# Kernel tuning notes

Hardware: AMD Instinct MI355X
Metric: run time of the kernel (lower is better)

The kernel has to match this reference:

```python
import jax, jax.numpy as jnp
import numpy as np

A, B, S, AD, H, NH = 8, 32768, 128, 16, 64, 4
D = H // NH  # attend_dim = 16
MAX_ACTION = 1.0


def setup_inputs() -> dict:
    key = jax.random.key(0)
    ks = jax.random.split(key, 16)
    sc = 0.05
    return {
        'states': jax.random.normal(ks[0], (A, B, S), jnp.float32),
        'actions': jax.random.normal(ks[1], (A, B, AD), jnp.float32),
        'Ws': jax.random.normal(ks[2], (S, H), jnp.float32) * sc,
        'bs': jnp.zeros((H,), jnp.float32),
        'We': jax.random.normal(ks[3], (S + AD, H), jnp.float32) * sc,
        'be': jnp.zeros((H,), jnp.float32),
        'Wk': jax.random.normal(ks[4], (NH, H, D), jnp.float32) * sc,
        'Wsel': jax.random.normal(ks[5], (NH, H, D), jnp.float32) * sc,
        'Wv': jax.random.normal(ks[6], (NH, H, D), jnp.float32) * sc,
        'bv': jnp.zeros((NH, D), jnp.float32),
        'W1': jax.random.normal(ks[7], (2 * H, H), jnp.float32) * sc,
        'b1': jnp.zeros((H,), jnp.float32),
        'W2': jax.random.normal(ks[8], (H, 1), jnp.float32) * sc,
        'b2': jnp.zeros((1,), jnp.float32),
    }


def reference(states, actions, Ws, bs, We, be, Wk, Wsel, Wv, bv, W1, b1, W2, b2):
    # per-agent encoders (shared params, as in the torch module)
    s_enc = jax.nn.relu(jnp.einsum('abs,sh->abh', states, Ws) + bs)          # [A,B,H]
    sa = jnp.concatenate([states, actions / MAX_ACTION], axis=-1)            # [A,B,S+AD]
    sa_enc = jax.nn.relu(jnp.einsum('abi,ih->abh', sa, We) + be)             # [A,B,H]

    # per-head keys / values / selectors (n = head axis)
    keys = jnp.einsum('abh,nhd->nabd', sa_enc, Wk)                           # [NH,A,B,D]
    vals = jax.nn.relu(jnp.einsum('abh,nhd->nabd', sa_enc, Wv) + bv[:, None, None, :])
    sel = jnp.einsum('abh,nhd->nabd', s_enc, Wsel)                           # [NH,A,B,D]

    # exclude-self attention over agents == masked softmax over agent axis j
    logits = jnp.einsum('nibd,njbd->nibj', sel, keys) / jnp.sqrt(jnp.float32(D))
    self_mask = jnp.eye(A, dtype=bool)                                       # [A(i),A(j)]
    logits = jnp.where(self_mask[None, :, None, :], -1e9, logits)
    w = jax.nn.softmax(logits, axis=-1)                                      # [NH,A,B,A]
    other = jnp.einsum('nibj,njbd->nibd', w, vals)                           # [NH,A,B,D]
    other_cat = jnp.transpose(other, (1, 2, 0, 3)).reshape(A, B, NH * D)     # [A,B,H]

    critic_in = jnp.concatenate([sa_enc, other_cat], axis=-1)                # [A,B,2H]
    h = jax.nn.relu(jnp.einsum('abi,ih->abh', critic_in, W1) + b1)
    q = jnp.einsum('abh,ho->abo', h, W2) + b2                                # [A,B,1]
    return q
```

## Files before the change

### kernel.cpp

```cpp
#include <hip/hip_runtime.h>
#include <hip/hip_bf16.h>

#define A_N 8
#define B_N 32768
#define S_N 128
#define AD_N 16

typedef __attribute__((ext_vector_type(8))) short short8;
typedef __attribute__((ext_vector_type(4))) float floatx4;

#define MFMA16(a, b, c) __builtin_amdgcn_mfma_f32_16x16x32_bf16(a, b, c, 0, 0, 0)

__device__ __forceinline__ short f2bf(float f) {
    __hip_bfloat16 h = __float2bfloat16(f);
    return *reinterpret_cast<short*>(&h);
}
__device__ __forceinline__ float bf2f(short s) {
    return __uint_as_float(((unsigned)(unsigned short)s) << 16);
}
__device__ __forceinline__ void pk2(short8& r, int i, float a, float b) {
    __hip_bfloat162 p = __float22bfloat162_rn(make_float2(a, b));
    short2 s = *reinterpret_cast<short2*>(&p);
    r[i] = s.x; r[i + 1] = s.y;
}
__device__ __forceinline__ short8 cvt8(float4 x0, float4 x1) {
    short8 r;
    pk2(r, 0, x0.x, x0.y); pk2(r, 2, x0.z, x0.w);
    pk2(r, 4, x1.x, x1.y); pk2(r, 6, x1.z, x1.w);
    return r;
}
__device__ __forceinline__ void wait_lgkm() {
    asm volatile("s_waitcnt lgkmcnt(0)" ::: "memory");
}
__device__ __forceinline__ void lds_barrier() {
    asm volatile("s_waitcnt lgkmcnt(0)\ns_barrier" ::: "memory");
}

#define W_TOTAL 41472
#define OFF_Ws 10240
#define OFF_Wk 18944
#define OFF_Wsel 23552
#define OFF_Wv 28160
#define OFF_W1 32768

__global__ void prep_weights(const float* __restrict__ Ws, const float* __restrict__ We,
                             const float* __restrict__ Wk, const float* __restrict__ Wsel,
                             const float* __restrict__ Wv, const float* __restrict__ W1,
                             short* __restrict__ w) {
    int idx = blockIdx.x * 256 + threadIdx.x;
    if (idx >= W_TOTAL) return;
    float v;
    if (idx < OFF_Ws)        { int n = idx / 160, k = idx % 160; v = (k < 144) ? We[k * 64 + n] : 0.f; }
    else if (idx < OFF_Wk)   { int i = idx - OFF_Ws;  int n = i / 136, k = i % 136; v = (k < 128) ? Ws[k * 64 + n] : 0.f; }
    else if (idx < OFF_Wsel) { int i = idx - OFF_Wk;  int n = i / 72,  k = i % 72;  v = (k < 64) ? Wk[(n >> 4) * 1024 + k * 16 + (n & 15)] : 0.f; }
    else if (idx < OFF_Wv)   { int i = idx - OFF_Wsel;int n = i / 72,  k = i % 72;  v = (k < 64) ? Wsel[(n >> 4) * 1024 + k * 16 + (n & 15)] : 0.f; }
    else if (idx < OFF_W1)   { int i = idx - OFF_Wv;  int n = i / 72,  k = i % 72;  v = (k < 64) ? Wv[(n >> 4) * 1024 + k * 16 + (n & 15)] : 0.f; }
    else                     { int i = idx - OFF_W1;  int n = i / 136, k = i % 136; v = (k < 128) ? W1[k * 64 + n] : 0.f; }
    w[idx] = f2bf(v);
}

#define ST 72
#define OFF_Eb 41472
#define OFF_Tb 50688
#define OFF_Kb 59904
#define OFF_Vb 69120
#define SMEM_TOT 78336

#define TILES 4

__global__ __launch_bounds__(512, 2)
void attention_critic_mfma(
    const float* __restrict__ states, const float* __restrict__ actions,
    const float* __restrict__ bs, const float* __restrict__ be,
    const float* __restrict__ bv, const float* __restrict__ b1,
    const float* __restrict__ W2, const float* __restrict__ b2,
    const short* __restrict__ wts, float* __restrict__ out)
{
    __shared__ __align__(16) short smem[SMEM_TOT];
    short* lWe   = smem;
    short* lWs   = smem + OFF_Ws;
    short* lWk   = smem + OFF_Wk;
    short* lWsel = smem + OFF_Wsel;
    short* lWv   = smem + OFF_Wv;
    short* lW1   = smem + OFF_W1;
    short* Eb    = smem + OFF_Eb;
    short* Tb    = smem + OFF_Tb;
    short* Kb    = smem + OFF_Kb;
    short* Vb    = smem + OFF_Vb;

    const int tid  = threadIdx.x;
    const int wv   = tid >> 6;
    const int lane = tid & 63;
    const int lq   = lane >> 4;
    const int ln   = lane & 15;
    const int rA   = wv * 16 + ln;
    const int bbase = blockIdx.x * (TILES * 16);

    for (int c = wv; c < 81; c += 8) {
        const unsigned int* g = reinterpret_cast<const unsigned int*>(wts + c * 512) + lane * 4;
        __builtin_amdgcn_global_load_lds(g, reinterpret_cast<unsigned int*>(smem + c * 512), 16, 0, 0);
    }

    const float* srow = states  + ((long)wv * B_N + bbase + ln) * S_N;
    const float* arow = actions + ((long)wv * B_N + bbase + ln) * AD_N;

    float4 ps[8]; float4 pa[2];
    #pragma unroll
    for (int s = 0; s < 4; ++s) {
        ps[2 * s]     = *reinterpret_cast<const float4*>(srow + s * 32 + lq * 8);
        ps[2 * s + 1] = *reinterpret_cast<const float4*>(srow + s * 32 + lq * 8 + 4);
    }
    if (lq < 2) {
        pa[0] = *reinterpret_cast<const float4*>(arow + lq * 8);
        pa[1] = *reinterpret_cast<const float4*>(arow + lq * 8 + 4);
    }
    __syncthreads();

    const floatx4 z = {0.f, 0.f, 0.f, 0.f};

    #pragma unroll 1
    for (int t = 0; t < TILES; ++t) {
        const int b0 = bbase + t * 16;

        floatx4 accE[4] = {z, z, z, z};
        floatx4 accS[4] = {z, z, z, z};
        #pragma unroll
        for (int s = 0; s < 4; ++s) {
            const int kk = s * 32 + lq * 8;
            short8 af = cvt8(ps[2 * s], ps[2 * s + 1]);
            #pragma unroll
            for (int nt = 0; nt < 4; ++nt) {
                short8 bE = *reinterpret_cast<const short8*>(lWe + (nt * 16 + ln) * 160 + kk);
                short8 bS = *reinterpret_cast<const short8*>(lWs + (nt * 16 + ln) * 136 + kk);
                accE[nt] = MFMA16(af, bE, accE[nt]);
                accS[nt] = MFMA16(af, bS, accS[nt]);
            }
        }
        {
            const int kk = 128 + lq * 8;
            short8 af = {0, 0, 0, 0, 0, 0, 0, 0};
            if (lq < 2) af = cvt8(pa[0], pa[1]);
            #pragma unroll
            for (int nt = 0; nt < 4; ++nt) {
                short8 bE = *reinterpret_cast<const short8*>(lWe + (nt * 16 + ln) * 160 + kk);
                accE[nt] = MFMA16(af, bE, accE[nt]);
            }
        }

        if (t + 1 < TILES) {
            srow += 16 * S_N; arow += 16 * AD_N;
            #pragma unroll
            for (int s = 0; s < 4; ++s) {
                ps[2 * s]     = *reinterpret_cast<const float4*>(srow + s * 32 + lq * 8);
                ps[2 * s + 1] = *reinterpret_cast<const float4*>(srow + s * 32 + lq * 8 + 4);
            }
            if (lq < 2) {
                pa[0] = *reinterpret_cast<const float4*>(arow + lq * 8);
                pa[1] = *reinterpret_cast<const float4*>(arow + lq * 8 + 4);
            }
        }

        #pragma unroll
        for (int nt = 0; nt < 4; ++nt) {
            const int col = nt * 16 + ln;
            const float bE = be[col], bS = bs[col];
            #pragma unroll
            for (int i = 0; i < 4; ++i) {
                const int row = wv * 16 + lq * 4 + i;
                Eb[row * ST + col] = f2bf(fmaxf(accE[nt][i] + bE, 0.f));
                Tb[row * ST + col] = f2bf(fmaxf(accS[nt][i] + bS, 0.f));
            }
        }
        wait_lgkm();

        floatx4 accSel[4] = {z, z, z, z};
        #pragma unroll
        for (int s = 0; s < 2; ++s) {
            short8 af = *reinterpret_cast<const short8*>(Tb + rA * ST + s * 32 + lq * 8);
            #pragma unroll
            for (int nt = 0; nt < 4; ++nt)
                accSel[nt] = MFMA16(af, *reinterpret_cast<const short8*>(lWsel + (nt * 16 + ln) * 72 + s * 32 + lq * 8), accSel[nt]);
        }
        #pragma unroll
        for (int nt = 0; nt < 4; ++nt)
            #pragma unroll
            for (int i = 0; i < 4; ++i)
                Tb[(wv * 16 + lq * 4 + i) * ST + nt * 16 + ln] = f2bf(accSel[nt][i]);

        floatx4 accK[4] = {z, z, z, z}, accV[4] = {z, z, z, z};
        #pragma unroll
        for (int s = 0; s < 2; ++s) {
            short8 af = *reinterpret_cast<const short8*>(Eb + rA * ST + s * 32 + lq * 8);
            #pragma unroll
            for (int nt = 0; nt < 4; ++nt) {
                accK[nt] = MFMA16(af, *reinterpret_cast<const short8*>(lWk + (nt * 16 + ln) * 72 + s * 32 + lq * 8), accK[nt]);
                accV[nt] = MFMA16(af, *reinterpret_cast<const short8*>(lWv + (nt * 16 + ln) * 72 + s * 32 + lq * 8), accV[nt]);
            }
        }
        #pragma unroll
        for (int nt = 0; nt < 4; ++nt) {
            const int col = nt * 16 + ln;
            const float bV = bv[col];
            #pragma unroll
            for (int i = 0; i < 4; ++i) {
                const int row = wv * 16 + lq * 4 + i;
                Kb[row * ST + col] = f2bf(accK[nt][i]);
                Vb[row * ST + col] = f2bf(fmaxf(accV[nt][i] + bV, 0.f));
            }
        }
        lds_barrier();

        {
            const int r3 = tid >> 2, hn = tid & 3;
            const int a3 = r3 >> 4, bl3 = r3 & 15;
            const int co = hn * 16;
            float selv[16];
            short8 s0 = *reinterpret_cast<const short8*>(Tb + r3 * ST + co);
            short8 s1 = *reinterpret_cast<const short8*>(Tb + r3 * ST + co + 8);
            #pragma unroll
            for (int d = 0; d < 8; ++d) { selv[d] = bf2f(s0[d]); selv[d + 8] = bf2f(s1[d]); }
            float lg[8];
            #pragma unroll
            for (int j = 0; j < 8; ++j) {
                const int rj = j * 16 + bl3;
                short8 k0 = *reinterpret_cast<const short8*>(Kb + rj * ST + co);
                short8 k1 = *reinterpret_cast<const short8*>(Kb + rj * ST + co + 8);
                float acc = 0.f;
                #pragma unroll
                for (int d = 0; d < 8; ++d) acc += selv[d] * bf2f(k0[d]) + selv[d + 8] * bf2f(k1[d]);
                lg[j] = (j == a3) ? -1e9f : acc * 0.25f;
            }
            float m = lg[0];
            #pragma unroll
            for (int j = 1; j < 8; ++j) m = fmaxf(m, lg[j]);
            float e[8], ssum = 0.f;
            #pragma unroll
            for (int j = 0; j < 8; ++j) { e[j] = __expf(lg[j] - m); ssum += e[j]; }
            const float inv = 1.f / ssum;
            float oth[16];
            #pragma unroll
            for (int d = 0; d < 16; ++d) oth[d] = 0.f;
            #pragma unroll
            for (int j = 0; j < 8; ++j) {
                const float wj = e[j] * inv;
                const int rj = j * 16 + bl3;
                short8 v0 = *reinterpret_cast<const short8*>(Vb + rj * ST + co);
                short8 v1 = *reinterpret_cast<const short8*>(Vb + rj * ST + co + 8);
                #pragma unroll
                for (int d = 0; d < 8; ++d) { oth[d] += wj * bf2f(v0[d]); oth[d + 8] += wj * bf2f(v1[d]); }
            }
            short8 o0, o1;
            #pragma unroll
            for (int d = 0; d < 8; ++d) { o0[d] = f2bf(oth[d]); o1[d] = f2bf(oth[d + 8]); }
            *reinterpret_cast<short8*>(Tb + r3 * ST + co)     = o0;
            *reinterpret_cast<short8*>(Tb + r3 * ST + co + 8) = o1;
        }
        wait_lgkm();

        floatx4 accH[4] = {z, z, z, z};
        #pragma unroll
        for (int s = 0; s < 4; ++s) {
            short8 af = (s < 2)
                ? *reinterpret_cast<const short8*>(Eb + rA * ST + s * 32 + lq * 8)
                : *reinterpret_cast<const short8*>(Tb + rA * ST + (s - 2) * 32 + lq * 8);
            #pragma unroll
            for (int nt = 0; nt < 4; ++nt)
                accH[nt] = MFMA16(af, *reinterpret_cast<const short8*>(lW1 + (nt * 16 + ln) * 136 + s * 32 + lq * 8), accH[nt]);
        }
        float p0 = 0.f, p1 = 0.f, p2 = 0.f, p3 = 0.f;
        #pragma unroll
        for (int nt = 0; nt < 4; ++nt) {
            const int col = nt * 16 + ln;
            const float w2v = W2[col], bb = b1[col];
            p0 += fmaxf(accH[nt][0] + bb, 0.f) * w2v;
            p1 += fmaxf(accH[nt][1] + bb, 0.f) * w2v;
            p2 += fmaxf(accH[nt][2] + bb, 0.f) * w2v;
            p3 += fmaxf(accH[nt][3] + bb, 0.f) * w2v;
        }
        #pragma unroll
        for (int mk = 1; mk < 16; mk <<= 1) {
            p0 += __shfl_xor(p0, mk, 64);
            p1 += __shfl_xor(p1, mk, 64);
            p2 += __shfl_xor(p2, mk, 64);
            p3 += __shfl_xor(p3, mk, 64);
        }
        if (ln == 0) {
            const float b2v = b2[0];
            float pr[4] = {p0, p1, p2, p3};
            #pragma unroll
            for (int i = 0; i < 4; ++i)
                out[(long)wv * B_N + b0 + lq * 4 + i] = pr[i] + b2v;
        }
        lds_barrier();
    }
}

extern "C" void kernel_launch(void* const* d_in, const int* in_sizes, int n_in,
                              void* d_out, int out_size, void* d_ws, size_t ws_size,
                              hipStream_t stream) {
    const float* states  = (const float*)d_in[0];
    const float* actions = (const float*)d_in[1];
    const float* Ws      = (const float*)d_in[2];
    const float* bs      = (const float*)d_in[3];
    const float* We      = (const float*)d_in[4];
    const float* be      = (const float*)d_in[5];
    const float* Wk      = (const float*)d_in[6];
    const float* Wsel    = (const float*)d_in[7];
    const float* Wv      = (const float*)d_in[8];
    const float* bv      = (const float*)d_in[9];
    const float* W1      = (const float*)d_in[10];
    const float* b1      = (const float*)d_in[11];
    const float* W2      = (const float*)d_in[12];
    const float* b2      = (const float*)d_in[13];
    short* wts = (short*)d_ws;
    float* out = (float*)d_out;

    prep_weights<<<(W_TOTAL + 255) / 256, 256, 0, stream>>>(Ws, We, Wk, Wsel, Wv, W1, wts);
    attention_critic_mfma<<<B_N / (TILES * 16), 512, 0, stream>>>(
        states, actions, bs, be, bv, b1, W2, b2, wts, out);
}
```

Before: 260.5 us.

## Remap rows so each wave holds all agents, removing block-wide barriers

Each wave's 16 rows now cover all 8 agents for 2 batch items, instead of 16 batch items of one agent. The attention step then reads only that wave's own K/V/sel rows, so the two s_barrier calls per tile become per-wave lgkm waits. The We row stride in LDS is also padded from 160 to 168, likely to reduce LDS bank conflicts. The cost is scattered global loads and stores, since each row now touches a different agent's memory region, giving less contiguous access per wave.

```diff
diff --git a/kernel.cpp b/kernel.cpp
--- a/kernel.cpp
+++ b/kernel.cpp
@@ -32,16 +32,13 @@
 __device__ __forceinline__ void wait_lgkm() {
     asm volatile("s_waitcnt lgkmcnt(0)" ::: "memory");
 }
-__device__ __forceinline__ void lds_barrier() {
-    asm volatile("s_waitcnt lgkmcnt(0)\ns_barrier" ::: "memory");
-}
-
-#define W_TOTAL 41472
-#define OFF_Ws 10240
-#define OFF_Wk 18944
-#define OFF_Wsel 23552
-#define OFF_Wv 28160
-#define OFF_W1 32768
+
+#define OFF_Ws 10752
+#define OFF_Wk 19456
+#define OFF_Wsel 24064
+#define OFF_Wv 28672
+#define OFF_W1 33280
+#define W_TOTAL 41984
 
 __global__ void prep_weights(const float* __restrict__ Ws, const float* __restrict__ We,
                              const float* __restrict__ Wk, const float* __restrict__ Wsel,
@@ -50,7 +47,7 @@
     int idx = blockIdx.x * 256 + threadIdx.x;
     if (idx >= W_TOTAL) return;
     float v;
-    if (idx < OFF_Ws)        { int n = idx / 160, k = idx % 160; v = (k < 144) ? We[k * 64 + n] : 0.f; }
+    if (idx < OFF_Ws)        { int n = idx / 168, k = idx % 168; v = (k < 144) ? We[k * 64 + n] : 0.f; }
     else if (idx < OFF_Wk)   { int i = idx - OFF_Ws;  int n = i / 136, k = i % 136; v = (k < 128) ? Ws[k * 64 + n] : 0.f; }
     else if (idx < OFF_Wsel) { int i = idx - OFF_Wk;  int n = i / 72,  k = i % 72;  v = (k < 64) ? Wk[(n >> 4) * 1024 + k * 16 + (n & 15)] : 0.f; }
     else if (idx < OFF_Wv)   { int i = idx - OFF_Wsel;int n = i / 72,  k = i % 72;  v = (k < 64) ? Wsel[(n >> 4) * 1024 + k * 16 + (n & 15)] : 0.f; }
@@ -60,11 +57,11 @@
 }
 
 #define ST 72
-#define OFF_Eb 41472
-#define OFF_Tb 50688
-#define OFF_Kb 59904
-#define OFF_Vb 69120
-#define SMEM_TOT 78336
+#define OFF_Eb 41984
+#define OFF_Tb 51200
+#define OFF_Kb 60416
+#define OFF_Vb 69632
+#define SMEM_TOT 78848
 
 #define TILES 4
 
@@ -96,13 +93,15 @@
     const int rA   = wv * 16 + ln;
     const int bbase = blockIdx.x * (TILES * 16);
 
-    for (int c = wv; c < 81; c += 8) {
+    for (int c = wv; c < 82; c += 8) {
         const unsigned int* g = reinterpret_cast<const unsigned int*>(wts + c * 512) + lane * 4;
         __builtin_amdgcn_global_load_lds(g, reinterpret_cast<unsigned int*>(smem + c * 512), 16, 0, 0);
     }
 
-    const float* srow = states  + ((long)wv * B_N + bbase + ln) * S_N;
-    const float* arow = actions + ((long)wv * B_N + bbase + ln) * AD_N;
+    const int aA  = ln & 7;
+    const int blA = ln >> 3;
+    const float* srow = states  + ((long)aA * B_N + bbase + wv * 2 + blA) * S_N;
+    const float* arow = actions + ((long)aA * B_N + bbase + wv * 2 + blA) * AD_N;
 
     float4 ps[8]; float4 pa[2];
     #pragma unroll
@@ -130,7 +129,7 @@
             short8 af = cvt8(ps[2 * s], ps[2 * s + 1]);
             #pragma unroll
             for (int nt = 0; nt < 4; ++nt) {
-                short8 bE = *reinterpret_cast<const short8*>(lWe + (nt * 16 + ln) * 160 + kk);
+                short8 bE = *reinterpret_cast<const short8*>(lWe + (nt * 16 + ln) * 168 + kk);
                 short8 bS = *reinterpret_cast<const short8*>(lWs + (nt * 16 + ln) * 136 + kk);
                 accE[nt] = MFMA16(af, bE, accE[nt]);
                 accS[nt] = MFMA16(af, bS, accS[nt]);
@@ -142,7 +141,7 @@
             if (lq < 2) af = cvt8(pa[0], pa[1]);
             #pragma unroll
             for (int nt = 0; nt < 4; ++nt) {
-                short8 bE = *reinterpret_cast<const short8*>(lWe + (nt * 16 + ln) * 160 + kk);
+                short8 bE = *reinterpret_cast<const short8*>(lWe + (nt * 16 + ln) * 168 + kk);
                 accE[nt] = MFMA16(af, bE, accE[nt]);
             }
         }
@@ -208,21 +207,23 @@
                 Vb[row * ST + col] = f2bf(fmaxf(accV[nt][i] + bV, 0.f));
             }
         }
-        lds_barrier();
+        wait_lgkm();
 
         {
-            const int r3 = tid >> 2, hn = tid & 3;
-            const int a3 = r3 >> 4, bl3 = r3 & 15;
+            const int r3 = lane >> 2;
+            const int hn = lane & 3;
+            const int a3 = r3 & 7;
+            const int rowbase = wv * 16 + (r3 & 8);
             const int co = hn * 16;
             float selv[16];
-            short8 s0 = *reinterpret_cast<const short8*>(Tb + r3 * ST + co);
-            short8 s1 = *reinterpret_cast<const short8*>(Tb + r3 * ST + co + 8);
+            short8 s0 = *reinterpret_cast<const short8*>(Tb + (wv * 16 + r3) * ST + co);
+            short8 s1 = *reinterpret_cast<const short8*>(Tb + (wv * 16 + r3) * ST + co + 8);
             #pragma unroll
             for (int d = 0; d < 8; ++d) { selv[d] = bf2f(s0[d]); selv[d + 8] = bf2f(s1[d]); }
             float lg[8];
             #pragma unroll
             for (int j = 0; j < 8; ++j) {
-                const int rj = j * 16 + bl3;
+                const int rj = rowbase + j;
                 short8 k0 = *reinterpret_cast<const short8*>(Kb + rj * ST + co);
                 short8 k1 = *reinterpret_cast<const short8*>(Kb + rj * ST + co + 8);
                 float acc = 0.f;
@@ -243,7 +244,7 @@
             #pragma unroll
             for (int j = 0; j < 8; ++j) {
                 const float wj = e[j] * inv;
-                const int rj = j * 16 + bl3;
+                const int rj = rowbase + j;
                 short8 v0 = *reinterpret_cast<const short8*>(Vb + rj * ST + co);
                 short8 v1 = *reinterpret_cast<const short8*>(Vb + rj * ST + co + 8);
                 #pragma unroll
@@ -252,8 +253,8 @@
             short8 o0, o1;
             #pragma unroll
             for (int d = 0; d < 8; ++d) { o0[d] = f2bf(oth[d]); o1[d] = f2bf(oth[d + 8]); }
-            *reinterpret_cast<short8*>(Tb + r3 * ST + co)     = o0;
-            *reinterpret_cast<short8*>(Tb + r3 * ST + co + 8) = o1;
+            *reinterpret_cast<short8*>(Tb + (wv * 16 + r3) * ST + co)     = o0;
+            *reinterpret_cast<short8*>(Tb + (wv * 16 + r3) * ST + co + 8) = o1;
         }
         wait_lgkm();
 
@@ -288,10 +289,11 @@
             const float b2v = b2[0];
             float pr[4] = {p0, p1, p2, p3};
             #pragma unroll
-            for (int i = 0; i < 4; ++i)
-                out[(long)wv * B_N + b0 + lq * 4 + i] = pr[i] + b2v;
-        }
-        lds_barrier();
+            for (int i = 0; i < 4; ++i) {
+                const int m = lq * 4 + i;
+                out[(long)(m & 7) * B_N + b0 + wv * 2 + (m >> 3)] = pr[i] + b2v;
+            }
+        }
     }
 }
 
```

After: 257.1 us. About the same (-1.3%).
